# Optimization experiments

Measured on AMD Instinct MI355X. Metric: run time of the kernel, lower is better.

## Reference

```python
import jax, jax.numpy as jnp
import numpy as np

N_LEVELS = 16
N_FEATS = 2
LOG2_T = 19
BASE_RES = 16.0
FINEST_RES = 512.0
N_POINTS = 1_000_000
HASH_MASK = np.uint32((1 << LOG2_T) - 1)
PRIME1 = np.uint32(2654435761)  # second spatial-hash prime (first is 1)


def setup_inputs() -> dict:
    key = jax.random.key(0)
    k1, k2 = jax.random.split(key)
    x = jax.random.uniform(k1, (N_POINTS, 2), dtype=jnp.float32)
    # nn.init.uniform_(w, -1e-4, 1e-4) per level, stacked: [L, T, F]
    embeddings = (jax.random.uniform(k2, (N_LEVELS, 2 ** LOG2_T, N_FEATS), dtype=jnp.float32) * 2.0 - 1.0) * 1e-4
    return {"x": x, "embeddings": embeddings}


def reference(x, embeddings):
    L = N_LEVELS
    n = x.shape[0]
    # per-level resolutions: floor(base * b**i)
    b = np.exp((np.log(FINEST_RES) - np.log(BASE_RES)) / (L - 1))
    res = np.floor(BASE_RES * b ** np.arange(L)).astype(np.float32)  # [L]
    res_j = jnp.asarray(res)

    pixels = x[None, :, :] * res_j[:, None, None]           # [L, n, 2]
    top_left = jnp.floor(pixels).astype(jnp.int32)          # [L, n, 2]
    offsets = jnp.array([[0, 0], [1, 0], [0, 1], [1, 1]], dtype=jnp.int32)
    box = top_left[:, :, None, :] + offsets[None, None]     # [L, n, 4, 2]
    box = jnp.clip(box, 0, res_j[:, None, None, None].astype(jnp.int32))

    # spatial hash: (c0*1 ^ c1*prime) & mask, with uint32 wraparound like torch int32
    c = box.astype(jnp.uint32)
    addr = ((c[..., 0] * np.uint32(1)) ^ (c[..., 1] * PRIME1)) & HASH_MASK  # [L, n, 4]
    addr = addr.astype(jnp.int32)

    # gather per-level corner features: [L, n, 4, F]
    feats = jax.vmap(lambda table, idx: table[idx])(embeddings, addr)

    # bilinear interpolation
    w = pixels - jnp.floor(pixels)                          # [L, n, 2]
    w0 = w[..., 0:1]
    w1 = w[..., 1:2]
    f0, f1, f2, f3 = feats[:, :, 0], feats[:, :, 1], feats[:, :, 2], feats[:, :, 3]
    f = (f0 * (1 - w0) + f1 * w0) * (1 - w1) + (f2 * (1 - w0) + f3 * w0) * w1  # [L, n, F]

    # concat levels along feature dim -> [n, L*F]
    return jnp.transpose(f, (1, 0, 2)).reshape(n, L * N_FEATS)
```

## Files before the change

### kernel.cpp

```cpp
#include <hip/hip_runtime.h>
#include <hip/hip_fp16.h>
#include <cmath>

#define NLVL 16
#define TSIZE (1u << 19)
#define HMASK ((1u << 19) - 1u)
#define PRIME1 2654435761u
#define FSCALE 1024.0f
#define FINV   (1.0f/1024.0f)

typedef float f32x4 __attribute__((ext_vector_type(4)));
typedef unsigned int       u32;
typedef unsigned long long u64;

struct Params {
    float rf[NLVL];
    int   ri[NLVL];
    int   base[NLVL];
    int   stride[NLVL];
};

__device__ __forceinline__ float2 h2f(u32 u) {
    __half2 h; __builtin_memcpy(&h, &u, 4);
    return __half22float2(h);
}

__global__ __launch_bounds__(256) void build_dense_h(
    const float2* __restrict__ emb, u32* __restrict__ dense, Params p)
{
    const int l  = blockIdx.y;
    const int cy = blockIdx.x;
    const int ri = p.ri[l];
    if (cy > ri) return;
    const unsigned hy = (unsigned)cy * PRIME1;
    const u64* tab = (const u64*)(emb + (size_t)l * TSIZE);
    u32* drow = dense + p.base[l] + (size_t)cy * p.stride[l];
    for (int cx = threadIdx.x; cx <= ri; cx += 256) {
        u64 raw = __builtin_nontemporal_load(tab + (((unsigned)cx ^ hy) & HMASK));
        float2 v; __builtin_memcpy(&v, &raw, 8);
        const u32 h0 = (u32)__half_as_ushort(__float2half_rn(v.x * FSCALE));
        const u32 h1 = (u32)__half_as_ushort(__float2half_rn(v.y * FSCALE));
        drow[cx] = h0 | (h1 << 16);
    }
}

__global__ __launch_bounds__(256) void hash_embed_h(
    const float2* __restrict__ x,
    const u32*    __restrict__ dense,
    float*        __restrict__ out,
    Params p, int n)
{
    __shared__ float lds[8 * 512];
    const int tid = threadIdx.x;
    const int i = blockIdx.x * 256 + tid;
    float2 xy = make_float2(0.f, 0.f);
    if (i < n) {
        u64 raw = __builtin_nontemporal_load((const u64*)(x + i));
        __builtin_memcpy(&xy, &raw, 8);
    }

    const long long total = (long long)n * 32;
    const long long base  = (long long)blockIdx.x * 8192;

    #pragma unroll
    for (int half = 0; half < 2; ++half) {
        u32 q0x[8], q0y[8], q1x[8], q1y[8];
        float w0v[8], w1v[8];
        int edge[8];
        #pragma unroll
        for (int j = 0; j < 8; ++j) {
            const int l = half * 8 + j;
            const float rf = p.rf[l];
            const int ri = p.ri[l];
            const float px = xy.x * rf, py = xy.y * rf;
            const float fx = floorf(px), fy = floorf(py);
            w0v[j] = px - fx;
            w1v[j] = py - fy;
            const int tx = (int)fx, ty = (int)fy;
            const int cx0 = min(tx, ri);
            const int cy0 = min(ty, ri);
            const int cy1 = min(ty + 1, ri);
            edge[j] = (cx0 == ri);
            const u32* tab = dense + p.base[l];
            uint2 a, b;
            __builtin_memcpy(&a, tab + cy0 * p.stride[l] + cx0, 8);
            __builtin_memcpy(&b, tab + cy1 * p.stride[l] + cx0, 8);
            q0x[j] = a.x; q0y[j] = a.y; q1x[j] = b.x; q1y[j] = b.y;
        }
        if (half == 1) __syncthreads();
        #pragma unroll
        for (int j = 0; j < 8; ++j) {
            const float w0 = w0v[j], w1 = w1v[j];
            const float u0 = 1.f - w0, u1 = 1.f - w1;
            const float2 e00 = h2f(q0x[j]);
            const float2 e01 = h2f(edge[j] ? q0x[j] : q0y[j]);
            const float2 e10 = h2f(q1x[j]);
            const float2 e11 = h2f(edge[j] ? q1x[j] : q1y[j]);
            const float g0 = ((e00.x*u0 + e01.x*w0)*u1 + (e10.x*u0 + e11.x*w0)*w1) * FINV;
            const float g1 = ((e00.y*u0 + e01.y*w0)*u1 + (e10.y*u0 + e11.y*w0)*w1) * FINV;
            const int idx = j * 512 + ((2 * tid) ^ (j << 1));
            lds[idx]     = g0;
            lds[idx + 1] = g1;
        }
        __syncthreads();

        #pragma unroll
        for (int it = 0; it < 4; ++it) {
            const int f  = (it * 256 + tid) * 4;
            const int p2 = f >> 4;
            const int kk = f & 15;
            const int lh = kk >> 1;
            const long long g = base + (long long)p2 * 32 + half * 16 + kk;
            if (g < total) {
                const int s0 = lh * 512       + ((2 * p2) ^ (lh << 1));
                const int s1 = (lh + 1) * 512 + ((2 * p2) ^ ((lh + 1) << 1));
                f32x4 v;
                v.x = lds[s0]; v.y = lds[s0 + 1];
                v.z = lds[s1]; v.w = lds[s1 + 1];
                __builtin_nontemporal_store(v, (f32x4*)(out + g));
            }
        }
    }
}

__global__ __launch_bounds__(256) void hash_embed_direct(
    const float2* __restrict__ x,
    const float2* __restrict__ emb,
    float* __restrict__ out,
    Params p, int n)
{
    __shared__ float2 lds[NLVL * 256];
    const int tid = threadIdx.x;
    const int i = blockIdx.x * 256 + tid;
    float2 xy = make_float2(0.f, 0.f);
    if (i < n) xy = x[i];

    #pragma unroll
    for (int half = 0; half < 2; ++half) {
        float2 f[32];
        float w0v[8], w1v[8];
        #pragma unroll
        for (int j = 0; j < 8; ++j) {
            const int l = half * 8 + j;
            const float rf = p.rf[l];
            const int ri = p.ri[l];
            const float px = xy.x * rf, py = xy.y * rf;
            const float fx = floorf(px), fy = floorf(py);
            w0v[j] = px - fx;
            w1v[j] = py - fy;
            const int tx = (int)fx, ty = (int)fy;
            const unsigned cx0 = (unsigned)min(tx, ri);
            const unsigned cy0 = (unsigned)min(ty, ri);
            const unsigned cx1 = (unsigned)min(tx + 1, ri);
            const unsigned cy1 = (unsigned)min(ty + 1, ri);
            const unsigned hy0 = cy0 * PRIME1;
            const unsigned hy1 = cy1 * PRIME1;
            const float2* tab = emb + (size_t)l * TSIZE;
            f[j*4+0] = tab[(cx0 ^ hy0) & HMASK];
            f[j*4+1] = tab[(cx1 ^ hy0) & HMASK];
            f[j*4+2] = tab[(cx0 ^ hy1) & HMASK];
            f[j*4+3] = tab[(cx1 ^ hy1) & HMASK];
        }
        #pragma unroll
        for (int j = 0; j < 8; ++j) {
            const int l = half * 8 + j;
            const float w0 = w0v[j], w1 = w1v[j];
            const float u0 = 1.f - w0, u1 = 1.f - w1;
            const float2 f0 = f[j*4+0], f1 = f[j*4+1], f2 = f[j*4+2], f3 = f[j*4+3];
            const float g0 = (f0.x*u0 + f1.x*w0)*u1 + (f2.x*u0 + f3.x*w0)*w1;
            const float g1 = (f0.y*u0 + f1.y*w0)*u1 + (f2.y*u0 + f3.y*w0)*w1;
            lds[l * 256 + tid] = make_float2(g0, g1);
        }
    }
    __syncthreads();

    const float* lf = (const float*)lds;
    const long long total = (long long)n * 32;
    const long long base = (long long)blockIdx.x * 8192;
    #pragma unroll
    for (int it = 0; it < 8; ++it) {
        const int k = (it * 256 + tid) * 4;
        if (base + k < total) {
            const int p2 = k >> 5;
            const int l0 = (k & 31) >> 1;
            float4 v;
            v.x = lf[(l0 * 256 + p2) * 2 + 0];
            v.y = lf[(l0 * 256 + p2) * 2 + 1];
            v.z = lf[((l0 + 1) * 256 + p2) * 2 + 0];
            v.w = lf[((l0 + 1) * 256 + p2) * 2 + 1];
            *(float4*)(out + base + k) = v;
        }
    }
}

extern "C" void kernel_launch(void* const* d_in, const int* in_sizes, int n_in,
                              void* d_out, int out_size, void* d_ws, size_t ws_size,
                              hipStream_t stream) {
    const float2* x = (const float2*)d_in[0];
    const float2* emb = (const float2*)d_in[1];
    float* out = (float*)d_out;
    const int n = in_sizes[0] / 2;

    Params p;
    int off = 0;
    const double b = std::exp((std::log(512.0) - std::log(16.0)) / 15.0);
    for (int l = 0; l < NLVL; ++l) {
        const double r = std::floor(16.0 * std::pow(b, (double)l));
        p.rf[l] = (float)r;
        p.ri[l] = (int)r;
        p.stride[l] = p.ri[l] + 2;
        p.base[l] = off;
        off += (p.ri[l] + 1) * (p.ri[l] + 2);
    }
    const size_t need = (size_t)off * sizeof(u32);

    const int grid = (n + 255) / 256;
    if (ws_size >= need) {
        build_dense_h<<<dim3(513, 16), 256, 0, stream>>>(emb, (u32*)d_ws, p);
        hash_embed_h<<<grid, 256, 0, stream>>>(x, (const u32*)d_ws, out, p, n);
    } else {
        hash_embed_direct<<<grid, 256, 0, stream>>>(x, emb, out, p, n);
    }
}
```

Baseline: 239.6 us.

## Bucket-sort points spatially before dense-grid gather to improve cache locality

Adds a counting sort of the input points into 128x128 spatial buckets (histogram with atomics, a single-block scan, and an atomic scatter). The main gather kernel then processes points in bucket order and writes each 32-float output row directly to the point's original index. The goal is locality: neighbouring threads touch nearby dense-table entries, which should cut cache misses on the fine levels. In exchange it adds three extra kernel passes plus a memset, global atomics, and scattered output row writes in place of the earlier LDS-transposed coalesced stores.

```diff
diff --git a/kernel.cpp b/kernel.cpp
--- a/kernel.cpp
+++ b/kernel.cpp
@@ -8,6 +8,8 @@
 #define PRIME1 2654435761u
 #define FSCALE 1024.0f
 #define FINV   (1.0f/1024.0f)
+#define NBUCK_1D 128
+#define NBUCK (NBUCK_1D * NBUCK_1D)
 
 typedef float f32x4 __attribute__((ext_vector_type(4)));
 typedef unsigned int       u32;
@@ -23,6 +25,12 @@
 __device__ __forceinline__ float2 h2f(u32 u) {
     __half2 h; __builtin_memcpy(&h, &u, 4);
     return __half22float2(h);
+}
+
+__device__ __forceinline__ int bucket_of(float2 xy) {
+    int bx = min(NBUCK_1D - 1, max(0, (int)(xy.x * (float)NBUCK_1D)));
+    int by = min(NBUCK_1D - 1, max(0, (int)(xy.y * (float)NBUCK_1D)));
+    return by * NBUCK_1D + bx;
 }
 
 __global__ __launch_bounds__(256) void build_dense_h(
@@ -44,23 +52,78 @@
     }
 }
 
-__global__ __launch_bounds__(256) void hash_embed_h(
-    const float2* __restrict__ x,
+__global__ __launch_bounds__(256) void hist_k(
+    const float2* __restrict__ x, u32* __restrict__ counts, int n)
+{
+    const int i = blockIdx.x * 256 + threadIdx.x;
+    if (i >= n) return;
+    u64 raw = __builtin_nontemporal_load((const u64*)(x + i));
+    float2 xy; __builtin_memcpy(&xy, &raw, 8);
+    atomicAdd(&counts[bucket_of(xy)], 1u);
+}
+
+__global__ __launch_bounds__(1024) void scan16k(
+    const u32* __restrict__ counts, u32* __restrict__ offs, u32* __restrict__ cursor)
+{
+    __shared__ u32 wsum[16];
+    const int t = threadIdx.x;
+    u32 v[16]; u32 s = 0;
+    #pragma unroll
+    for (int k = 0; k < 16; ++k) { v[k] = counts[t * 16 + k]; s += v[k]; }
+    u32 inc = s;
+    #pragma unroll
+    for (int d = 1; d < 64; d <<= 1) {
+        u32 tt = __shfl_up(inc, d);
+        if ((t & 63) >= d) inc += tt;
+    }
+    if ((t & 63) == 63) wsum[t >> 6] = inc;
+    __syncthreads();
+    if (t < 16) {
+        u32 w = wsum[t];
+        u32 wi = w;
+        #pragma unroll
+        for (int d = 1; d < 16; d <<= 1) {
+            u32 tt = __shfl_up(wi, d);
+            if (t >= d) wi += tt;
+        }
+        wsum[t] = wi - w;
+    }
+    __syncthreads();
+    u32 run = wsum[t >> 6] + (inc - s);
+    #pragma unroll
+    for (int k = 0; k < 16; ++k) {
+        offs[t * 16 + k]   = run;
+        cursor[t * 16 + k] = run;
+        run += v[k];
+    }
+}
+
+__global__ __launch_bounds__(256) void scatter_k(
+    const float2* __restrict__ x, u32* __restrict__ cursor,
+    float2* __restrict__ sx, u32* __restrict__ oidx, int n)
+{
+    const int i = blockIdx.x * 256 + threadIdx.x;
+    if (i >= n) return;
+    u64 raw = __builtin_nontemporal_load((const u64*)(x + i));
+    float2 xy; __builtin_memcpy(&xy, &raw, 8);
+    const u32 pos = atomicAdd(&cursor[bucket_of(xy)], 1u);
+    sx[pos] = xy;
+    oidx[pos] = (u32)i;
+}
+
+__global__ __launch_bounds__(256) void hash_embed_sorted(
+    const float2* __restrict__ sx,
+    const u32*    __restrict__ oidx,
     const u32*    __restrict__ dense,
     float*        __restrict__ out,
     Params p, int n)
 {
-    __shared__ float lds[8 * 512];
-    const int tid = threadIdx.x;
-    const int i = blockIdx.x * 256 + tid;
-    float2 xy = make_float2(0.f, 0.f);
-    if (i < n) {
-        u64 raw = __builtin_nontemporal_load((const u64*)(x + i));
-        __builtin_memcpy(&xy, &raw, 8);
-    }
-
-    const long long total = (long long)n * 32;
-    const long long base  = (long long)blockIdx.x * 8192;
+    const int i = blockIdx.x * 256 + threadIdx.x;
+    if (i >= n) return;
+    u64 raw = __builtin_nontemporal_load((const u64*)(sx + i));
+    float2 xy; __builtin_memcpy(&xy, &raw, 8);
+    const u32 oi = __builtin_nontemporal_load(oidx + i);
+    float* dst = out + (size_t)oi * 32;
 
     #pragma unroll
     for (int half = 0; half < 2; ++half) {
@@ -87,6 +150,68 @@
             __builtin_memcpy(&b, tab + cy1 * p.stride[l] + cx0, 8);
             q0x[j] = a.x; q0y[j] = a.y; q1x[j] = b.x; q1y[j] = b.y;
         }
+        float g[16];
+        #pragma unroll
+        for (int j = 0; j < 8; ++j) {
+            const float w0 = w0v[j], w1 = w1v[j];
+            const float u0 = 1.f - w0, u1 = 1.f - w1;
+            const float2 e00 = h2f(q0x[j]);
+            const float2 e01 = h2f(edge[j] ? q0x[j] : q0y[j]);
+            const float2 e10 = h2f(q1x[j]);
+            const float2 e11 = h2f(edge[j] ? q1x[j] : q1y[j]);
+            g[j*2+0] = ((e00.x*u0 + e01.x*w0)*u1 + (e10.x*u0 + e11.x*w0)*w1) * FINV;
+            g[j*2+1] = ((e00.y*u0 + e01.y*w0)*u1 + (e10.y*u0 + e11.y*w0)*w1) * FINV;
+        }
+        #pragma unroll
+        for (int q = 0; q < 4; ++q) {
+            f32x4 v; v.x = g[q*4+0]; v.y = g[q*4+1]; v.z = g[q*4+2]; v.w = g[q*4+3];
+            __builtin_nontemporal_store(v, (f32x4*)(dst + half * 16 + q * 4));
+        }
+    }
+}
+
+__global__ __launch_bounds__(256) void hash_embed_h(
+    const float2* __restrict__ x,
+    const u32*    __restrict__ dense,
+    float*        __restrict__ out,
+    Params p, int n)
+{
+    __shared__ float lds[8 * 512];
+    const int tid = threadIdx.x;
+    const int i = blockIdx.x * 256 + tid;
+    float2 xy = make_float2(0.f, 0.f);
+    if (i < n) {
+        u64 raw = __builtin_nontemporal_load((const u64*)(x + i));
+        __builtin_memcpy(&xy, &raw, 8);
+    }
+    const long long total = (long long)n * 32;
+    const long long base  = (long long)blockIdx.x * 8192;
+
+    #pragma unroll
+    for (int half = 0; half < 2; ++half) {
+        u32 q0x[8], q0y[8], q1x[8], q1y[8];
+        float w0v[8], w1v[8];
+        int edge[8];
+        #pragma unroll
+        for (int j = 0; j < 8; ++j) {
+            const int l = half * 8 + j;
+            const float rf = p.rf[l];
+            const int ri = p.ri[l];
+            const float px = xy.x * rf, py = xy.y * rf;
+            const float fx = floorf(px), fy = floorf(py);
+            w0v[j] = px - fx;
+            w1v[j] = py - fy;
+            const int tx = (int)fx, ty = (int)fy;
+            const int cx0 = min(tx, ri);
+            const int cy0 = min(ty, ri);
+            const int cy1 = min(ty + 1, ri);
+            edge[j] = (cx0 == ri);
+            const u32* tab = dense + p.base[l];
+            uint2 a, b;
+            __builtin_memcpy(&a, tab + cy0 * p.stride[l] + cx0, 8);
+            __builtin_memcpy(&b, tab + cy1 * p.stride[l] + cx0, 8);
+            q0x[j] = a.x; q0y[j] = a.y; q1x[j] = b.x; q1y[j] = b.y;
+        }
         if (half == 1) __syncthreads();
         #pragma unroll
         for (int j = 0; j < 8; ++j) {
@@ -103,21 +228,20 @@
             lds[idx + 1] = g1;
         }
         __syncthreads();
-
         #pragma unroll
         for (int it = 0; it < 4; ++it) {
             const int f  = (it * 256 + tid) * 4;
             const int p2 = f >> 4;
             const int kk = f & 15;
             const int lh = kk >> 1;
-            const long long g = base + (long long)p2 * 32 + half * 16 + kk;
-            if (g < total) {
+            const long long gaddr = base + (long long)p2 * 32 + half * 16 + kk;
+            if (gaddr < total) {
                 const int s0 = lh * 512       + ((2 * p2) ^ (lh << 1));
                 const int s1 = (lh + 1) * 512 + ((2 * p2) ^ ((lh + 1) << 1));
                 f32x4 v;
                 v.x = lds[s0]; v.y = lds[s0 + 1];
                 v.z = lds[s1]; v.w = lds[s1 + 1];
-                __builtin_nontemporal_store(v, (f32x4*)(out + g));
+                __builtin_nontemporal_store(v, (f32x4*)(out + gaddr));
             }
         }
     }
@@ -212,12 +336,35 @@
         p.base[l] = off;
         off += (p.ri[l] + 1) * (p.ri[l] + 2);
     }
-    const size_t need = (size_t)off * sizeof(u32);
+    const size_t D = (size_t)off;
+    const size_t need_dense = D * sizeof(u32);
+
+    const size_t c_counts = D;
+    const size_t c_offs   = c_counts + NBUCK;
+    const size_t c_cursor = c_offs + NBUCK;
+    const size_t c_oidx   = c_cursor + NBUCK;
+    size_t c_sx           = c_oidx + (size_t)n;
+    if (c_sx & 1) ++c_sx;
+    const size_t need_sort = (c_sx + 2 * (size_t)n) * sizeof(u32);
 
     const int grid = (n + 255) / 256;
-    if (ws_size >= need) {
-        build_dense_h<<<dim3(513, 16), 256, 0, stream>>>(emb, (u32*)d_ws, p);
-        hash_embed_h<<<grid, 256, 0, stream>>>(x, (const u32*)d_ws, out, p, n);
+    u32* base = (u32*)d_ws;
+
+    if (ws_size >= need_sort) {
+        u32* counts = base + c_counts;
+        u32* offs   = base + c_offs;
+        u32* cursor = base + c_cursor;
+        u32* oidx   = base + c_oidx;
+        float2* sx  = (float2*)(base + c_sx);
+        hipMemsetAsync(counts, 0, NBUCK * sizeof(u32), stream);
+        build_dense_h<<<dim3(513, 16), 256, 0, stream>>>(emb, base, p);
+        hist_k<<<grid, 256, 0, stream>>>(x, counts, n);
+        scan16k<<<1, 1024, 0, stream>>>(counts, offs, cursor);
+        scatter_k<<<grid, 256, 0, stream>>>(x, cursor, sx, oidx, n);
+        hash_embed_sorted<<<grid, 256, 0, stream>>>(sx, oidx, base, out, p, n);
+    } else if (ws_size >= need_dense) {
+        build_dense_h<<<dim3(513, 16), 256, 0, stream>>>(emb, base, p);
+        hash_embed_h<<<grid, 256, 0, stream>>>(x, base, out, p, n);
     } else {
         hash_embed_direct<<<grid, 256, 0, stream>>>(x, emb, out, p, n);
     }
```

Measured after the change: 636.3 us. +165.6%, slower.

## Pack vertical corner pairs into dense table and issue all level loads upfront

Applied to the files above, without the earlier changes.

The dense precomputed table now stores, for each cell, both the row-y and row-y+1 half-precision features in a uint2. Each point can then fetch all four bilinear corners with a single 16-byte load per level instead of two 8-byte loads. All 16 levels' loads are issued before any interpolation, with a sched_barrier, so more memory requests are in flight. This doubles the dense table size and build work, and raises register use for holding 16 uint4 values, which may lower occupancy.

```diff
diff --git a/kernel.cpp b/kernel.cpp
--- a/kernel.cpp
+++ b/kernel.cpp
@@ -25,28 +25,35 @@
     return __half22float2(h);
 }
 
-__global__ __launch_bounds__(256) void build_dense_h(
-    const float2* __restrict__ emb, u32* __restrict__ dense, Params p)
+__global__ __launch_bounds__(256) void build_dense_q(
+    const float2* __restrict__ emb, uint2* __restrict__ dense, Params p)
 {
     const int l  = blockIdx.y;
-    const int cy = blockIdx.x;
+    const int r  = blockIdx.x;
     const int ri = p.ri[l];
-    if (cy > ri) return;
-    const unsigned hy = (unsigned)cy * PRIME1;
+    if (r > ri) return;
+    const unsigned hy0 = (unsigned)r * PRIME1;
+    const unsigned hy1 = (unsigned)min(r + 1, ri) * PRIME1;
     const u64* tab = (const u64*)(emb + (size_t)l * TSIZE);
-    u32* drow = dense + p.base[l] + (size_t)cy * p.stride[l];
+    uint2* drow = dense + p.base[l] + (size_t)r * p.stride[l];
     for (int cx = threadIdx.x; cx <= ri; cx += 256) {
-        u64 raw = __builtin_nontemporal_load(tab + (((unsigned)cx ^ hy) & HMASK));
-        float2 v; __builtin_memcpy(&v, &raw, 8);
-        const u32 h0 = (u32)__half_as_ushort(__float2half_rn(v.x * FSCALE));
-        const u32 h1 = (u32)__half_as_ushort(__float2half_rn(v.y * FSCALE));
-        drow[cx] = h0 | (h1 << 16);
-    }
-}
-
-__global__ __launch_bounds__(256) void hash_embed_h(
+        u64 raw0 = __builtin_nontemporal_load(tab + (((unsigned)cx ^ hy0) & HMASK));
+        u64 raw1 = __builtin_nontemporal_load(tab + (((unsigned)cx ^ hy1) & HMASK));
+        float2 v0, v1;
+        __builtin_memcpy(&v0, &raw0, 8);
+        __builtin_memcpy(&v1, &raw1, 8);
+        uint2 e;
+        e.x = (u32)__half_as_ushort(__float2half_rn(v0.x * FSCALE))
+            | ((u32)__half_as_ushort(__float2half_rn(v0.y * FSCALE)) << 16);
+        e.y = (u32)__half_as_ushort(__float2half_rn(v1.x * FSCALE))
+            | ((u32)__half_as_ushort(__float2half_rn(v1.y * FSCALE)) << 16);
+        drow[cx] = e;
+    }
+}
+
+__global__ __launch_bounds__(256) void hash_embed_q(
     const float2* __restrict__ x,
-    const u32*    __restrict__ dense,
+    const uint2*  __restrict__ dense,
     float*        __restrict__ out,
     Params p, int n)
 {
@@ -59,43 +66,43 @@
         __builtin_memcpy(&xy, &raw, 8);
     }
 
+    uint4 q[NLVL];
+    float w0v[NLVL], w1v[NLVL];
+    u32 edgemask = 0;
+
+    #pragma unroll
+    for (int l = 0; l < NLVL; ++l) {
+        const float rf = p.rf[l];
+        const int ri = p.ri[l];
+        const float px = xy.x * rf, py = xy.y * rf;
+        const float fx = floorf(px), fy = floorf(py);
+        w0v[l] = px - fx;
+        w1v[l] = py - fy;
+        const int tx = (int)fx, ty = (int)fy;
+        const int cx0 = min(tx, ri);
+        const int cy0 = min(ty, ri);
+        edgemask |= (u32)(cx0 == ri) << l;
+        const uint2* a = dense + p.base[l] + cy0 * p.stride[l] + cx0;
+        __builtin_memcpy(&q[l], a, 16);
+    }
+    __builtin_amdgcn_sched_barrier(0);
+
     const long long total = (long long)n * 32;
     const long long base  = (long long)blockIdx.x * 8192;
 
     #pragma unroll
     for (int half = 0; half < 2; ++half) {
-        u32 q0x[8], q0y[8], q1x[8], q1y[8];
-        float w0v[8], w1v[8];
-        int edge[8];
+        if (half == 1) __syncthreads();
         #pragma unroll
         for (int j = 0; j < 8; ++j) {
             const int l = half * 8 + j;
-            const float rf = p.rf[l];
-            const int ri = p.ri[l];
-            const float px = xy.x * rf, py = xy.y * rf;
-            const float fx = floorf(px), fy = floorf(py);
-            w0v[j] = px - fx;
-            w1v[j] = py - fy;
-            const int tx = (int)fx, ty = (int)fy;
-            const int cx0 = min(tx, ri);
-            const int cy0 = min(ty, ri);
-            const int cy1 = min(ty + 1, ri);
-            edge[j] = (cx0 == ri);
-            const u32* tab = dense + p.base[l];
-            uint2 a, b;
-            __builtin_memcpy(&a, tab + cy0 * p.stride[l] + cx0, 8);
-            __builtin_memcpy(&b, tab + cy1 * p.stride[l] + cx0, 8);
-            q0x[j] = a.x; q0y[j] = a.y; q1x[j] = b.x; q1y[j] = b.y;
-        }
-        if (half == 1) __syncthreads();
-        #pragma unroll
-        for (int j = 0; j < 8; ++j) {
-            const float w0 = w0v[j], w1 = w1v[j];
+            const float w0 = w0v[l], w1 = w1v[l];
             const float u0 = 1.f - w0, u1 = 1.f - w1;
-            const float2 e00 = h2f(q0x[j]);
-            const float2 e01 = h2f(edge[j] ? q0x[j] : q0y[j]);
-            const float2 e10 = h2f(q1x[j]);
-            const float2 e11 = h2f(edge[j] ? q1x[j] : q1y[j]);
+            const bool ed = (edgemask >> l) & 1u;
+            const float2 e00 = h2f(q[l].x);
+            const float2 e10 = h2f(q[l].y);
+            const float2 e01 = h2f(ed ? q[l].x : q[l].z);
+            const float2 e11 = h2f(ed ? q[l].y : q[l].w);
             const float g0 = ((e00.x*u0 + e01.x*w0)*u1 + (e10.x*u0 + e11.x*w0)*w1) * FINV;
             const float g1 = ((e00.y*u0 + e01.y*w0)*u1 + (e10.y*u0 + e11.y*w0)*w1) * FINV;
             const int idx = j * 512 + ((2 * tid) ^ (j << 1));
@@ -212,12 +219,12 @@
         p.base[l] = off;
         off += (p.ri[l] + 1) * (p.ri[l] + 2);
     }
-    const size_t need = (size_t)off * sizeof(u32);
+    const size_t need = (size_t)off * sizeof(uint2);
 
     const int grid = (n + 255) / 256;
     if (ws_size >= need) {
-        build_dense_h<<<dim3(513, 16), 256, 0, stream>>>(emb, (u32*)d_ws, p);
-        hash_embed_h<<<grid, 256, 0, stream>>>(x, (const u32*)d_ws, out, p, n);
+        build_dense_q<<<dim3(513, 16), 256, 0, stream>>>(emb, (uint2*)d_ws, p);
+        hash_embed_q<<<grid, 256, 0, stream>>>(x, (const uint2*)d_ws, out, p, n);
     } else {
         hash_embed_direct<<<grid, 256, 0, stream>>>(x, emb, out, p, n);
     }
```

After: 231.2 us. -3.5%, faster.
